# Kernel tuning notes

Measured on AMD Instinct MI355X. Metric: run time of the kernel, lower is better.

Reference implementation:

```python
import jax, jax.numpy as jnp
import numpy as np

N, E, G = 10000, 160000, 64      # nodes, edges, graphs
IN, H, L = 128, 128, 14          # in_channels, hidden, num GENConv layers
EPS_LN = 1e-5                    # torch LayerNorm eps
EPS_MSG = 1e-7                   # GENConv message eps


def layer_norm(x, g, b):
    mu = jnp.mean(x, axis=-1, keepdims=True)
    v = jnp.var(x, axis=-1, keepdims=True)
    return (x - mu) * jax.lax.rsqrt(v + EPS_LN) * g + b


def gen_conv(h, src, dst, t, sc, W1, b1, mg, mb, W2, b2):
    # message: relu(x_j) + eps  (no edge_attr)
    msg = jax.nn.relu(h[src]) + EPS_MSG                      # [E, H]
    # softmax aggregation over edges sharing a destination, per feature
    z = msg * t
    mx = jax.ops.segment_max(z, dst, num_segments=N)         # [N, H]
    mx = jnp.where(jnp.isfinite(mx), mx, 0.0)
    e = jnp.exp(z - mx[dst])
    ssum = jax.ops.segment_sum(e, dst, num_segments=N)
    alpha = e / (ssum[dst] + 1e-16)
    agg = jax.ops.segment_sum(msg * alpha, dst, num_segments=N)  # [N, H]
    # MessageNorm: normalize(agg) * ||h|| * scale
    agg = agg / jnp.maximum(jnp.linalg.norm(agg, axis=-1, keepdims=True), 1e-12)
    agg = agg * jnp.linalg.norm(h, axis=-1, keepdims=True) * sc
    out = h + agg
    # MLP [H, 2H, H] with LayerNorm + ReLU between (dropout off in eval)
    z1 = layer_norm(out @ W1 + b1, mg, mb)
    return jax.nn.relu(z1) @ W2 + b2


def setup_inputs() -> dict:
    key = jax.random.key(0)
    ks = jax.random.split(key, 8)
    s = 0.05
    x = jax.random.normal(ks[0], (N, IN), jnp.float32)
    edge_index = jax.random.randint(ks[1], (2, E), 0, N, dtype=jnp.int64)
    batch = jnp.sort(jax.random.randint(ks[2], (N,), 0, G, dtype=jnp.int64))
    enc_W = jax.random.normal(ks[3], (IN, H), jnp.float32) * s
    enc_b = jnp.zeros((H,), jnp.float32)
    ln_g = jnp.ones((L, H), jnp.float32)
    ln_b = jnp.zeros((L, H), jnp.float32)
    t = jnp.ones((L,), jnp.float32)         # learnable softmax temperature
    scale = jnp.ones((L,), jnp.float32)     # learnable MsgNorm scale
    W1 = jax.random.normal(ks[4], (L, H, 2 * H), jnp.float32) * s
    b1 = jnp.zeros((L, 2 * H), jnp.float32)
    mg = jnp.ones((L, 2 * H), jnp.float32)
    mb = jnp.zeros((L, 2 * H), jnp.float32)
    W2 = jax.random.normal(ks[5], (L, 2 * H, H), jnp.float32) * s
    b2 = jnp.zeros((L, H), jnp.float32)
    fn_g = jnp.ones((H,), jnp.float32)
    fn_b = jnp.zeros((H,), jnp.float32)
    return dict(x=x, edge_index=edge_index, batch=batch, enc_W=enc_W, enc_b=enc_b,
                ln_g=ln_g, ln_b=ln_b, t=t, scale=scale, W1=W1, b1=b1, mg=mg, mb=mb,
                W2=W2, b2=b2, fn_g=fn_g, fn_b=fn_b)


def reference(x, edge_index, batch, enc_W, enc_b, ln_g, ln_b, t, scale,
              W1, b1, mg, mb, W2, b2, fn_g, fn_b):
    src, dst = edge_index[0], edge_index[1]
    h = x @ enc_W + enc_b
    for i in range(L):  # DeepGCNLayer 'res+': x + conv(act(norm(x)))
        r = jax.nn.leaky_relu(layer_norm(h, ln_g[i], ln_b[i]), 0.01)
        h = h + gen_conv(r, src, dst, t[i], scale[i],
                         W1[i], b1[i], mg[i], mb[i], W2[i], b2[i])
    h = jax.nn.leaky_relu(layer_norm(h, fn_g, fn_b), 0.01)
    # global_mean_pool (fin_map is unused in the original forward)
    cnt = jax.ops.segment_sum(jnp.ones((N,), h.dtype), batch, num_segments=G)
    gf = jax.ops.segment_sum(h, batch, num_segments=G) / jnp.maximum(cnt, 1.0)[:, None]
    return gf
```

## Files before the change

### kernel.cpp

```cpp
#include <hip/hip_runtime.h>
#include <cstdint>
#include <cstddef>


#define BT 512

typedef __attribute__((ext_vector_type(8))) short bf16x8;
typedef __attribute__((ext_vector_type(4))) float f32x4;

__device__ inline float bf2f(ushort u) {
    union { uint i; float f; } v;
    v.i = (uint)u << 16;
    return v.f;
}
__device__ inline ushort f2bf(float f) {
    union { float f; uint i; } v;
    v.f = f;
    return (ushort)((v.i + 0x7fffu + ((v.i >> 16) & 1u)) >> 16);
}
__device__ inline uint f2bf2(float a, float b) {
    return (uint)f2bf(a) | ((uint)f2bf(b) << 16);
}

__device__ inline float wave_sum_f(float v) {
#pragma unroll
    for (int off = 32; off > 0; off >>= 1) v += __shfl_xor(v, off, 64);
    return v;
}

__global__ void setup_kernel(const float* __restrict__ x, ushort* __restrict__ xb,
                             const int* __restrict__ dst, int* __restrict__ deg,
                             const int* __restrict__ batch, int* __restrict__ gstart,
                             int total, int N, int E, int G) {
    int idx = blockIdx.x * blockDim.x + threadIdx.x;
    if (idx >= total) return;
    xb[idx] = f2bf(x[idx]);
    if (idx < E) atomicAdd(&deg[dst[idx]], 1);
    if (idx < N) {
        int bb = batch[idx];
        if (idx == 0)
            for (int g = 0; g <= bb; g++) gstart[g] = 0;
        else {
            int pb = batch[idx - 1];
            for (int g = pb + 1; g <= bb; g++) gstart[g] = idx;
        }
        if (idx == N - 1)
            for (int g = bb + 1; g <= G; g++) gstart[g] = N;
    }
}

__global__ __launch_bounds__(1024) void scan_kernel(const int* __restrict__ deg,
                                                    int* __restrict__ offs,
                                                    int* __restrict__ cursor, int N) {
    __shared__ int part[1024];
    int tid = threadIdx.x;
    int CH = (N + 1023) / 1024;
    int base = tid * CH;
    int s = 0;
    for (int i = 0; i < CH; i++) {
        int idx = base + i;
        if (idx < N) s += deg[idx];
    }
    part[tid] = s;
    __syncthreads();
    for (int off = 1; off < 1024; off <<= 1) {
        int v = (tid >= off) ? part[tid - off] : 0;
        __syncthreads();
        part[tid] += v;
        __syncthreads();
    }
    int run = (tid == 0) ? 0 : part[tid - 1];
    for (int i = 0; i < CH; i++) {
        int idx = base + i;
        if (idx < N) {
            offs[idx] = run;
            cursor[idx] = run;
            run += deg[idx];
        }
    }
    if (tid == 1023) offs[N] = part[1023];
}

__global__ void scatter_kernel(const int* __restrict__ src, const int* __restrict__ dst,
                               int* __restrict__ cursor, int* __restrict__ esrc, int E) {
    int e = blockIdx.x * blockDim.x + threadIdx.x;
    if (e < E) {
        int d = dst[e];
        int pos = atomicAdd(&cursor[d], 1);
        esrc[pos] = src[e];
    }
}

__global__ __launch_bounds__(256) void prep_kernel(const float* __restrict__ W1,
                                                   const float* __restrict__ W2,
                                                   const float* __restrict__ encW,
                                                   ushort* __restrict__ W1t,
                                                   ushort* __restrict__ W2t,
                                                   ushort* __restrict__ encWt, int L) {
    __shared__ float tile[32][33];
    int z = blockIdx.z;
    const float* in;
    ushort* out;
    int R, C;
    if (z < L) {
        in = W1 + (size_t)z * 32768; out = W1t + (size_t)z * 32768; R = 128; C = 256;
    } else if (z < 2 * L) {
        int i = z - L;
        in = W2 + (size_t)i * 32768; out = W2t + (size_t)i * 32768; R = 256; C = 128;
    } else {
        in = encW; out = encWt; R = 128; C = 128;
    }
    int r0 = blockIdx.y * 32, c0 = blockIdx.x * 32;
    if (r0 >= R || c0 >= C) return;
    int tx = threadIdx.x & 31, ty = threadIdx.x >> 5;
    for (int i = ty; i < 32; i += 8) tile[i][tx] = in[(size_t)(r0 + i) * C + c0 + tx];
    __syncthreads();
    for (int i = ty; i < 32; i += 8)
        out[(size_t)(c0 + i) * R + r0 + tx] = f2bf(tile[tx][i]);
}

__device__ __forceinline__ void agg_stage_v13(const ushort* __restrict__ rin,
                                              const int* __restrict__ offs,
                                              const int* __restrict__ esrc,
                                              const float* __restrict__ rnbuf,
                                              float tv, float sv, int row0,
                                              int w, int l, uint (*AsU)[68]) {
    const uint2* rin2 = (const uint2*)rin;
    int nd0 = row0 + 2 * w;
    int half = l >> 5, li = l & 31;
    int a0 = offs[nd0], a1 = offs[nd0 + 1], a2 = offs[nd0 + 2];
    int eb[2] = {a0, a1};
    int dg[2] = {a1 - a0, a2 - a1};

    float s[2][4] = {}, W[2][4] = {};
    int mxdeg = max(dg[0], dg[1]);

#pragma unroll 1
    for (int base = 0; base < mxdeg; base += 64) {
        int rem0 = min(dg[0] - base, 64);
        int rem1 = min(dg[1] - base, 64);
        int idx0 = (rem0 > 0 && l < rem0) ? esrc[eb[0] + base + l] : 0;
        int idx1 = (rem1 > 0 && l < rem1) ? esrc[eb[1] + base + l] : 0;
        int it = (max(rem0, rem1) + 7) >> 3;
#pragma unroll 1
        for (int i = 0; i < it; i++) {
            int j0 = i * 8 + half;
            uint2 rv[2][4];
            bool vl[2][4];
#pragma unroll
            for (int c = 0; c < 4; c++) {
                int j = j0 + 2 * c;
                vl[0][c] = j < rem0;
                vl[1][c] = j < rem1;
                int sn0 = __shfl(idx0, j, 64);
                int sn1 = __shfl(idx1, j, 64);
                if (vl[0][c]) rv[0][c] = rin2[(size_t)sn0 * 32 + li];
                if (vl[1][c]) rv[1][c] = rin2[(size_t)sn1 * 32 + li];
            }
#pragma unroll
            for (int k = 0; k < 2; k++)
#pragma unroll
                for (int c = 0; c < 4; c++) {
                    if (vl[k][c]) {
                        float f0 = bf2f((ushort)(rv[k][c].x & 0xffff));
                        float f1 = bf2f((ushort)(rv[k][c].x >> 16));
                        float f2 = bf2f((ushort)(rv[k][c].y & 0xffff));
                        float f3 = bf2f((ushort)(rv[k][c].y >> 16));
                        float g0 = fmaxf(f0, 0.f) + 1e-7f;
                        float g1 = fmaxf(f1, 0.f) + 1e-7f;
                        float g2 = fmaxf(f2, 0.f) + 1e-7f;
                        float g3 = fmaxf(f3, 0.f) + 1e-7f;
                        float p0 = __expf(g0 * tv);
                        float p1 = __expf(g1 * tv);
                        float p2 = __expf(g2 * tv);
                        float p3 = __expf(g3 * tv);
                        s[k][0] += p0; W[k][0] += g0 * p0;
                        s[k][1] += p1; W[k][1] += g1 * p1;
                        s[k][2] += p2; W[k][2] += g2 * p2;
                        s[k][3] += p3; W[k][3] += g3 * p3;
                    }
                }
        }
    }

#pragma unroll
    for (int k = 0; k < 2; k++) {
#pragma unroll
        for (int f = 0; f < 4; f++) {
            s[k][f] += __shfl_xor(s[k][f], 32, 64);
            W[k][f] += __shfl_xor(W[k][f], 32, 64);
        }
        float agg[4], nsq = 0.f;
#pragma unroll
        for (int f = 0; f < 4; f++) {
            agg[f] = W[k][f] / (s[k][f] + 1e-16f);
            nsq += agg[f] * agg[f];
        }
#pragma unroll
        for (int off = 1; off < 32; off <<= 1) nsq += __shfl_xor(nsq, off, 64);
        int nd = nd0 + k;
        float fac = rnbuf[nd] * sv / fmaxf(sqrtf(nsq), 1e-12f);
        uint2 ru = rin2[(size_t)nd * 32 + li];
        if (half == 0) {
            uint2 o;
            o.x = f2bf2(bf2f((ushort)(ru.x & 0xffff)) + agg[0] * fac,
                        bf2f((ushort)(ru.x >> 16)) + agg[1] * fac);
            o.y = f2bf2(bf2f((ushort)(ru.y & 0xffff)) + agg[2] * fac,
                        bf2f((ushort)(ru.y >> 16)) + agg[3] * fac);
            *(uint2*)&AsU[2 * w + k][2 * li] = o;
        }
    }
}

__device__ __forceinline__ void gemm1_stage8(const ushort (*As)[136],
                                             const ushort* __restrict__ Bt,
                                             const float* __restrict__ bias,
                                             const float* __restrict__ mg,
                                             const float* __restrict__ mb,
                                             ushort (*z1s)[264],
                                             int w, int q, int ln,
                                             float (*pS)[16], float (*pQ)[16]) {
    f32x4 acc[2];
    acc[0] = (f32x4){0.f, 0.f, 0.f, 0.f};
    acc[1] = (f32x4){0.f, 0.f, 0.f, 0.f};
#pragma unroll
    for (int ks = 0; ks < 128; ks += 32) {
        bf16x8 a = *(const bf16x8*)&As[ln][ks + q * 8];
#pragma unroll
        for (int ct = 0; ct < 2; ct++) {
            bf16x8 bv = *(const bf16x8*)(Bt + (size_t)(w * 32 + ct * 16 + ln) * 128 + ks + q * 8);
            acc[ct] = __builtin_amdgcn_mfma_f32_16x16x32_bf16(a, bv, acc[ct], 0, 0, 0);
        }
    }
    float s1[4] = {0, 0, 0, 0}, s2[4] = {0, 0, 0, 0};
#pragma unroll
    for (int ct = 0; ct < 2; ct++)
#pragma unroll
        for (int r = 0; r < 4; r++) {
            float v = acc[ct][r] + bias[w * 32 + ct * 16 + ln];
            acc[ct][r] = v;
            s1[r] += v;
            s2[r] += v * v;
        }
#pragma unroll
    for (int off = 1; off < 16; off <<= 1)
#pragma unroll
        for (int r = 0; r < 4; r++) {
            s1[r] += __shfl_xor(s1[r], off, 64);
            s2[r] += __shfl_xor(s2[r], off, 64);
        }
    if (ln == 0)
#pragma unroll
        for (int r = 0; r < 4; r++) {
            pS[w][q * 4 + r] = s1[r];
            pQ[w][q * 4 + r] = s2[r];
        }
    __syncthreads();
#pragma unroll
    for (int r = 0; r < 4; r++) {
        int row = q * 4 + r;
        float S = 0.f, Q = 0.f;
#pragma unroll
        for (int ww = 0; ww < 8; ww++) {
            S += pS[ww][row];
            Q += pQ[ww][row];
        }
        float mu = S * (1.f / 256.f);
        float var = Q * (1.f / 256.f) - mu * mu;
        float rs = rsqrtf(var + 1e-5f);
#pragma unroll
        for (int ct = 0; ct < 2; ct++) {
            int col = w * 32 + ct * 16 + ln;
            float y = (acc[ct][r] - mu) * rs * mg[col] + mb[col];
            z1s[row][col] = f2bf(fmaxf(y, 0.f));
        }
    }
    __syncthreads();
}

template <int KD, bool RESID>
__device__ __forceinline__ void out_stage8(const ushort* __restrict__ Abase, int astr,
                                           const ushort* __restrict__ Bt,
                                           const float* __restrict__ bias,
                                           const float* __restrict__ lg,
                                           const float* __restrict__ lb,
                                           float* __restrict__ hbuf,
                                           ushort* __restrict__ rout,
                                           float* __restrict__ rnbuf,
                                           int row0, int w, int q, int ln,
                                           float (*pS)[16], float (*pQ)[16]) {
    f32x4 acc = (f32x4){0.f, 0.f, 0.f, 0.f};
    int col = w * 16 + ln;
#pragma unroll
    for (int ks = 0; ks < KD; ks += 32) {
        bf16x8 a = *(const bf16x8*)(Abase + ln * astr + ks + q * 8);
        bf16x8 bv = *(const bf16x8*)(Bt + (size_t)col * KD + ks + q * 8);
        acc = __builtin_amdgcn_mfma_f32_16x16x32_bf16(a, bv, acc, 0, 0, 0);
    }
    float s1[4], s2[4];
#pragma unroll
    for (int r = 0; r < 4; r++) {
        int row = q * 4 + r;
        float v = acc[r] + bias[col];
        if (RESID) v += hbuf[(size_t)(row0 + row) * 128 + col];
        hbuf[(size_t)(row0 + row) * 128 + col] = v;
        acc[r] = v;
        s1[r] = v;
        s2[r] = v * v;
    }
#pragma unroll
    for (int off = 1; off < 16; off <<= 1)
#pragma unroll
        for (int r = 0; r < 4; r++) {
            s1[r] += __shfl_xor(s1[r], off, 64);
            s2[r] += __shfl_xor(s2[r], off, 64);
        }
    if (ln == 0)
#pragma unroll
        for (int r = 0; r < 4; r++) {
            pS[w][q * 4 + r] = s1[r];
            pQ[w][q * 4 + r] = s2[r];
        }
    __syncthreads();
    float yv[4];
    float t2[4];
#pragma unroll
    for (int r = 0; r < 4; r++) {
        int row = q * 4 + r;
        float S = 0.f, Q = 0.f;
#pragma unroll
        for (int ww = 0; ww < 8; ww++) {
            S += pS[ww][row];
            Q += pQ[ww][row];
        }
        float mu = S * (1.f / 128.f);
        float var = Q * (1.f / 128.f) - mu * mu;
        float rs = rsqrtf(var + 1e-5f);
        float y = (acc[r] - mu) * rs * lg[col] + lb[col];
        y = y > 0.f ? y : 0.01f * y;
        yv[r] = y;
        t2[r] = y * y;
    }
#pragma unroll
    for (int off = 1; off < 16; off <<= 1)
#pragma unroll
        for (int r = 0; r < 4; r++) t2[r] += __shfl_xor(t2[r], off, 64);
    __syncthreads();
    if (ln == 0)
#pragma unroll
        for (int r = 0; r < 4; r++) pS[w][q * 4 + r] = t2[r];
    __syncthreads();
#pragma unroll
    for (int r = 0; r < 4; r++) {
        int row = q * 4 + r;
        float T = 0.f;
#pragma unroll
        for (int ww = 0; ww < 8; ww++) T += pS[ww][row];
        if (w == 0 && ln == 0) rnbuf[row0 + row] = sqrtf(T);
        rout[(size_t)(row0 + row) * 128 + col] = f2bf(yv[r]);
    }
}

__global__ __launch_bounds__(BT) void enc_kernel(const ushort* __restrict__ xb,
                                                 const ushort* __restrict__ encWt,
                                                 const float* __restrict__ encB,
                                                 const float* __restrict__ lg,
                                                 const float* __restrict__ lb,
                                                 float* __restrict__ h,
                                                 ushort* __restrict__ r,
                                                 float* __restrict__ rn, int N) {
    __shared__ __align__(16) ushort As[16][136];
    __shared__ float pS[8][16], pQ[8][16];
    uint(*AsU)[68] = (uint(*)[68])As;
    int tid = threadIdx.x, w = tid >> 6, l = tid & 63;
    int q = l >> 4, ln = l & 15;
    int row0 = blockIdx.x * 16;
    for (int idx = tid; idx < 16 * 64; idx += BT) {
        int row = idx >> 6, cl = idx & 63;
        AsU[row][cl] = ((const uint*)xb)[(size_t)(row0 + row) * 64 + cl];
    }
    __syncthreads();
    out_stage8<128, false>(&As[0][0], 136, encWt, encB, lg, lb, h, r, rn,
                           row0, w, q, ln, pS, pQ);
}

__global__ __launch_bounds__(BT) void layer_kernel(const ushort* __restrict__ rin,
                                                   ushort* __restrict__ rout,
                                                   const int* __restrict__ offs,
                                                   const int* __restrict__ esrc,
                                                   float* __restrict__ rn,
                                                   float* __restrict__ h,
                                                   const ushort* __restrict__ W1t,
                                                   const ushort* __restrict__ W2t,
                                                   const float* __restrict__ b1,
                                                   const float* __restrict__ mg,
                                                   const float* __restrict__ mb,
                                                   const float* __restrict__ b2,
                                                   const float* __restrict__ ng,
                                                   const float* __restrict__ nb,
                                                   const float* __restrict__ tptr,
                                                   const float* __restrict__ scptr,
                                                   int N) {
    __shared__ __align__(16) ushort As[16][136];
    __shared__ __align__(16) ushort z1s[16][264];
    __shared__ float pS[8][16], pQ[8][16];
    uint(*AsU)[68] = (uint(*)[68])As;
    int tid = threadIdx.x, w = tid >> 6, l = tid & 63;
    int q = l >> 4, ln = l & 15;
    int row0 = blockIdx.x * 16;
    float tv = *tptr, sv = *scptr;
    agg_stage_v13(rin, offs, esrc, rn, tv, sv, row0, w, l, AsU);
    __syncthreads();
    gemm1_stage8(As, W1t, b1, mg, mb, z1s, w, q, ln, pS, pQ);
    out_stage8<256, true>(&z1s[0][0], 264, W2t, b2, ng, nb, h, rout, rn,
                          row0, w, q, ln, pS, pQ);
}

__global__ __launch_bounds__(256) void pool_kernel(const ushort* __restrict__ rf,
                                                   const int* __restrict__ gstart,
                                                   float* __restrict__ out) {
    __shared__ float pb0[4][64], pb1[4][64];
    int g = blockIdx.x;
    int w = threadIdx.x >> 6, l = threadIdx.x & 63;
    int s = gstart[g], e = gstart[g + 1];
    float a0 = 0.f, a1 = 0.f;
    for (int n = s + w; n < e; n += 4) {
        uint rv = ((const uint*)rf)[(size_t)n * 64 + l];
        a0 += bf2f((ushort)(rv & 0xffff));
        a1 += bf2f((ushort)(rv >> 16));
    }
    pb0[w][l] = a0;
    pb1[w][l] = a1;
    __syncthreads();
    if (threadIdx.x < 64) {
        float t0 = pb0[0][l] + pb0[1][l] + pb0[2][l] + pb0[3][l];
        float t1 = pb1[0][l] + pb1[1][l] + pb1[2][l] + pb1[3][l];
        float inv = 1.f / fmaxf((float)(e - s), 1.f);
        out[g * 128 + 2 * l] = t0 * inv;
        out[g * 128 + 2 * l + 1] = t1 * inv;
    }
}

extern "C" void kernel_launch(void* const* d_in, const int* in_sizes, int n_in,
                              void* d_out, int out_size, void* d_ws, size_t ws_size,
                              hipStream_t stream) {
    const float* x     = (const float*)d_in[0];
    const int*   ei    = (const int*)d_in[1];
    const int*   batch = (const int*)d_in[2];
    const float* encW  = (const float*)d_in[3];
    const float* encB  = (const float*)d_in[4];
    const float* ln_g  = (const float*)d_in[5];
    const float* ln_b  = (const float*)d_in[6];
    const float* tArr  = (const float*)d_in[7];
    const float* scArr = (const float*)d_in[8];
    const float* W1    = (const float*)d_in[9];
    const float* b1    = (const float*)d_in[10];
    const float* mg    = (const float*)d_in[11];
    const float* mb    = (const float*)d_in[12];
    const float* W2    = (const float*)d_in[13];
    const float* b2    = (const float*)d_in[14];
    const float* fn_g  = (const float*)d_in[15];
    const float* fn_b  = (const float*)d_in[16];
    float* out = (float*)d_out;

    const int N = in_sizes[0] / 128;
    const int E = in_sizes[1] / 2;
    const int L = in_sizes[7];
    const int G = 64;

    const int* src = ei;
    const int* dst = ei + E;

    char* p = (char*)d_ws;
    auto alloc = [&](size_t bytes) -> void* {
        void* qp = (void*)p;
        p += (bytes + 255) & ~(size_t)255;
        return qp;
    };
    int*    deg    = (int*)alloc((size_t)N * 4);
    int*    offs   = (int*)alloc((size_t)(N + 1) * 4);
    int*    cursor = (int*)alloc((size_t)N * 4);
    int*    esrc   = (int*)alloc((size_t)E * 4);
    int*    gstart = (int*)alloc((size_t)(G + 1) * 4);
    float*  h      = (float*)alloc((size_t)N * 128 * 4);
    ushort* r0     = (ushort*)alloc((size_t)N * 128 * 2);
    ushort* r1     = (ushort*)alloc((size_t)N * 128 * 2);
    float*  rn     = (float*)alloc((size_t)N * 4);
    ushort* xb     = (ushort*)alloc((size_t)N * 128 * 2);
    ushort* W1t    = (ushort*)alloc((size_t)L * 32768 * 2);
    ushort* W2t    = (ushort*)alloc((size_t)L * 32768 * 2);
    ushort* encWt  = (ushort*)alloc((size_t)16384 * 2);

    (void)hipMemsetAsync(deg, 0, (size_t)N * 4, stream);

    setup_kernel<<<(N * 128 + 255) / 256, 256, 0, stream>>>(x, xb, dst, deg, batch,
                                                            gstart, N * 128, N, E, G);
    scan_kernel<<<1, 1024, 0, stream>>>(deg, offs, cursor, N);
    scatter_kernel<<<(E + 255) / 256, 256, 0, stream>>>(src, dst, cursor, esrc, E);
    prep_kernel<<<dim3(8, 8, 2 * L + 1), 256, 0, stream>>>(W1, W2, encW, W1t, W2t,
                                                           encWt, L);

    const int TILES = N / 16;

    enc_kernel<<<TILES, BT, 0, stream>>>(xb, encWt, encB, ln_g, ln_b, h, r0, rn, N);

    for (int i = 0; i < L; i++) {
        const ushort* rin = (i & 1) ? r1 : r0;
        ushort* rout = (i & 1) ? r0 : r1;
        const float* ng = (i < L - 1) ? (ln_g + (size_t)(i + 1) * 128) : fn_g;
        const float* nb = (i < L - 1) ? (ln_b + (size_t)(i + 1) * 128) : fn_b;
        layer_kernel<<<TILES, BT, 0, stream>>>(rin, rout, offs, esrc, rn, h,
                                               W1t + ((size_t)i << 15),
                                               W2t + ((size_t)i << 15),
                                               b1 + (size_t)i * 256,
                                               mg + (size_t)i * 256,
                                               mb + (size_t)i * 256,
                                               b2 + (size_t)i * 128,
                                               ng, nb, tArr + i, scArr + i, N);
    }

    const ushort* rf = ((L - 1) & 1) ? r0 : r1;
    pool_kernel<<<G, 256, 0, stream>>>(rf, gstart, out);
}
```

Baseline: 585.7 us.

## Schedule layer tiles by descending max degree and prefetch residual rows early

Adds a one-block kernel that computes each 16-node tile's maximum in-degree and ranks the tiles so the layer kernel processes the heaviest tiles first (a longest-job-first order that reduces tail imbalance). The layer kernel maps blockIdx through this order array. The aggregation stage also loads the residual row and norm for its two nodes before the edge loop instead of after it, hiding that latency. The cost is an O(T^2) ranking kernel run once, an extra indirection per block, and a loss of locality between consecutively scheduled tiles.

```diff
diff --git a/kernel.cpp b/kernel.cpp
--- a/kernel.cpp
+++ b/kernel.cpp
@@ -88,6 +88,28 @@
         int d = dst[e];
         int pos = atomicAdd(&cursor[d], 1);
         esrc[pos] = src[e];
+    }
+}
+
+__global__ __launch_bounds__(1024) void order_kernel(const int* __restrict__ offs,
+                                                     int* __restrict__ order, int T) {
+    __shared__ int wts[640];
+    int t = threadIdx.x;
+    if (t < T) {
+        int mx = 0, base = t * 16;
+#pragma unroll 1
+        for (int k = 0; k < 16; k++) mx = max(mx, offs[base + k + 1] - offs[base + k]);
+        wts[t] = mx;
+    }
+    __syncthreads();
+    if (t < T) {
+        int wv = wts[t], rank = 0;
+#pragma unroll 1
+        for (int j = 0; j < T; j++) {
+            int wj = wts[j];
+            if (wj > wv || (wj == wv && j < t)) rank++;
+        }
+        order[rank] = t;
     }
 }
 
@@ -119,7 +141,7 @@
         out[(size_t)(c0 + i) * R + r0 + tx] = f2bf(tile[tx][i]);
 }
 
-__device__ __forceinline__ void agg_stage_v13(const ushort* __restrict__ rin,
+__device__ __forceinline__ void agg_stage_v15(const ushort* __restrict__ rin,
                                               const int* __restrict__ offs,
                                               const int* __restrict__ esrc,
                                               const float* __restrict__ rnbuf,
@@ -131,6 +153,10 @@
     int a0 = offs[nd0], a1 = offs[nd0 + 1], a2 = offs[nd0 + 2];
     int eb[2] = {a0, a1};
     int dg[2] = {a1 - a0, a2 - a1};
+
+    uint2 ru0 = rin2[(size_t)nd0 * 32 + li];
+    uint2 ru1 = rin2[(size_t)(nd0 + 1) * 32 + li];
+    float rn0 = rnbuf[nd0], rn1 = rnbuf[nd0 + 1];
 
     float s[2][4] = {}, W[2][4] = {};
     int mxdeg = max(dg[0], dg[1]);
@@ -198,9 +224,9 @@
         }
 #pragma unroll
         for (int off = 1; off < 32; off <<= 1) nsq += __shfl_xor(nsq, off, 64);
-        int nd = nd0 + k;
-        float fac = rnbuf[nd] * sv / fmaxf(sqrtf(nsq), 1e-12f);
-        uint2 ru = rin2[(size_t)nd * 32 + li];
+        float rnv = (k == 0) ? rn0 : rn1;
+        uint2 ru = (k == 0) ? ru0 : ru1;
+        float fac = rnv * sv / fmaxf(sqrtf(nsq), 1e-12f);
         if (half == 0) {
             uint2 o;
             o.x = f2bf2(bf2f((ushort)(ru.x & 0xffff)) + agg[0] * fac,
@@ -367,7 +393,7 @@
                                                  const float* __restrict__ lg,
                                                  const float* __restrict__ lb,
                                                  float* __restrict__ h,
-                                                 ushort* __restrict__ r,
+                                                 ushort* __restrict__ rbuf,
                                                  float* __restrict__ rn, int N) {
     __shared__ __align__(16) ushort As[16][136];
     __shared__ float pS[8][16], pQ[8][16];
@@ -380,7 +406,7 @@
         AsU[row][cl] = ((const uint*)xb)[(size_t)(row0 + row) * 64 + cl];
     }
     __syncthreads();
-    out_stage8<128, false>(&As[0][0], 136, encWt, encB, lg, lb, h, r, rn,
+    out_stage8<128, false>(&As[0][0], 136, encWt, encB, lg, lb, h, rbuf, rn,
                            row0, w, q, ln, pS, pQ);
 }
 
@@ -388,6 +414,7 @@
                                                    ushort* __restrict__ rout,
                                                    const int* __restrict__ offs,
                                                    const int* __restrict__ esrc,
+                                                   const int* __restrict__ order,
                                                    float* __restrict__ rn,
                                                    float* __restrict__ h,
                                                    const ushort* __restrict__ W1t,
@@ -407,9 +434,9 @@
     uint(*AsU)[68] = (uint(*)[68])As;
     int tid = threadIdx.x, w = tid >> 6, l = tid & 63;
     int q = l >> 4, ln = l & 15;
-    int row0 = blockIdx.x * 16;
+    int row0 = order[blockIdx.x] * 16;
     float tv = *tptr, sv = *scptr;
-    agg_stage_v13(rin, offs, esrc, rn, tv, sv, row0, w, l, AsU);
+    agg_stage_v15(rin, offs, esrc, rn, tv, sv, row0, w, l, AsU);
     __syncthreads();
     gemm1_stage8(As, W1t, b1, mg, mb, z1s, w, q, ln, pS, pQ);
     out_stage8<256, true>(&z1s[0][0], 264, W2t, b2, ng, nb, h, rout, rn,
@@ -482,6 +509,7 @@
     int*    cursor = (int*)alloc((size_t)N * 4);
     int*    esrc   = (int*)alloc((size_t)E * 4);
     int*    gstart = (int*)alloc((size_t)(G + 1) * 4);
+    int*    order  = (int*)alloc((size_t)1024 * 4);
     float*  h      = (float*)alloc((size_t)N * 128 * 4);
     ushort* r0     = (ushort*)alloc((size_t)N * 128 * 2);
     ushort* r1     = (ushort*)alloc((size_t)N * 128 * 2);
@@ -501,6 +529,7 @@
                                                            encWt, L);
 
     const int TILES = N / 16;
+    order_kernel<<<1, 1024, 0, stream>>>(offs, order, TILES);
 
     enc_kernel<<<TILES, BT, 0, stream>>>(xb, encWt, encB, ln_g, ln_b, h, r0, rn, N);
 
@@ -509,7 +538,7 @@
         ushort* rout = (i & 1) ? r0 : r1;
         const float* ng = (i < L - 1) ? (ln_g + (size_t)(i + 1) * 128) : fn_g;
         const float* nb = (i < L - 1) ? (ln_b + (size_t)(i + 1) * 128) : fn_b;
-        layer_kernel<<<TILES, BT, 0, stream>>>(rin, rout, offs, esrc, rn, h,
+        layer_kernel<<<TILES, BT, 0, stream>>>(rin, rout, offs, esrc, order, rn, h,
                                                W1t + ((size_t)i << 15),
                                                W2t + ((size_t)i << 15),
                                                b1 + (size_t)i * 256,
```

Result: slower. 615.2 us (+5.0%).
